# Kernel tuning notes

Measured on AMD Instinct MI355X. Metric: run time of the kernel, lower is better.

## Reference

```python
import jax, jax.numpy as jnp
from jax import lax
import numpy as np

GAMMA = 0.25        # inv_temp
C_SCALE = 1.0       # spectral_scale
STRIDE = 8          # patch stride (== patch_size, non-overlapping)


def setup_inputs() -> dict:
    key = jax.random.key(0)
    ks = jax.random.split(key, 9)
    B, C, H = 1024, 3, 64
    D, NP, M, NH, R, P = 256, 64, 1024, 8, 32, 8
    return {
        "x": jax.random.normal(ks[0], (B, C, H, H), jnp.float32),
        "z": jax.random.normal(ks[1], (B, NP, D), jnp.float32),
        "encoder_weight": jax.random.normal(ks[2], (D, C, P, P), jnp.float32) * 0.05,
        "encoder_bias": jax.random.normal(ks[3], (D,), jnp.float32) * 0.05,
        "visible_bias": jax.random.normal(ks[4], (C, H, H), jnp.float32) * 0.05,
        "pos_bias": jax.random.normal(ks[5], (NP, D), jnp.float32) * 0.05,
        "memory_weight": jax.random.normal(ks[6], (D, M), jnp.float32) * 0.05,
        "W_Q": jax.random.normal(ks[7], (NH, R, D), jnp.float32) * 0.05,
        "W_K": jax.random.normal(ks[8], (NH, R, D), jnp.float32) * 0.05,
    }


def reference(x, z, encoder_weight, encoder_bias, visible_bias, pos_bias,
              memory_weight, W_Q, W_K):
    """E = 0.5||x||^2 + 0.5||z||^2 - Phi_coupling(x, z); returns (B,)."""
    B = x.shape[0]
    D = encoder_weight.shape[0]

    quad_x = 0.5 * jnp.sum(x * x, axis=(1, 2, 3))
    quad_z = 0.5 * jnp.sum(z * z, axis=(1, 2))

    # visible-bias coupling
    phi_vis = jnp.sum(visible_bias[None] * x, axis=(1, 2, 3))

    # conv encode: (B, D, gh, gw) -> (B, NP, D)
    enc = lax.conv_general_dilated(
        x, C_SCALE * encoder_weight, window_strides=(STRIDE, STRIDE),
        padding='VALID', dimension_numbers=('NCHW', 'OIHW', 'NCHW'))
    encoded = enc.reshape(B, D, -1).transpose(0, 2, 1)  # (B, NP, D)

    # enc_act = 'none' -> identity
    phi_enc = jnp.sum(encoded * z, axis=(1, 2))
    phi_bias = jnp.sum(z * encoder_bias, axis=(1, 2))
    phi_pos = jnp.sum(z * pos_bias[None], axis=(1, 2))

    # memory ReLU^2 term: (B, NP, M)
    mem_proj = jnp.einsum('bpd,dm->bpm', z, C_SCALE * memory_weight)
    phi_mem = jnp.sum(jnp.square(jax.nn.relu(mem_proj)), axis=(1, 2))

    # Hopfield attention logsumexp term
    Q = jnp.einsum('bpd,hrd->bhrp', z, C_SCALE * W_Q)  # (B, H, R, NP)
    K = jnp.einsum('bpd,hrd->bhrp', z, C_SCALE * W_K)
    A = jnp.einsum('bhdm,bhdn->bhmn', Q, K)            # (B, H, NP, NP)
    phi_att = jnp.sum(jax.scipy.special.logsumexp(GAMMA * A, axis=-1),
                      axis=(1, 2)) / GAMMA

    coupling = phi_vis + phi_enc + phi_bias + phi_pos + phi_mem + phi_att
    return quad_x + quad_z - coupling
```

## Files before the change

kernel.cpp:

```cpp
#include <hip/hip_runtime.h>
#include <hip/hip_bf16.h>

#define GAMMA 0.25f


typedef __attribute__((ext_vector_type(8))) short short8;
typedef __attribute__((ext_vector_type(4))) float f32x4;

__device__ __forceinline__ float dot4(float4 a, float4 b) {
  return fmaf(a.x, b.x, fmaf(a.y, b.y, fmaf(a.z, b.z, a.w * b.w)));
}

__device__ __forceinline__ void fma4(float4& a, float s, float4 w) {
  a.x = fmaf(s, w.x, a.x); a.y = fmaf(s, w.y, a.y);
  a.z = fmaf(s, w.z, a.z); a.w = fmaf(s, w.w, a.w);
}

__device__ __forceinline__ ushort f2bf(float f) {
  __hip_bfloat16 h = __float2bfloat16(f);
  return *reinterpret_cast<ushort*>(&h);
}

__device__ __forceinline__ float bf2f(ushort u) {
  union { unsigned int i; float f; } v;
  v.i = ((unsigned int)u) << 16;
  return v.f;
}

__device__ __forceinline__ float block_sum_256(float v, float* tmp) {
#pragma unroll
  for (int off = 32; off; off >>= 1) v += __shfl_down(v, off, 64);
  int w = threadIdx.x >> 6;
  if ((threadIdx.x & 63) == 0) tmp[w] = v;
  __syncthreads();
  return tmp[0] + tmp[1] + tmp[2] + tmp[3];
}

__global__ __launch_bounds__(256) void k_cvt_weights_v4(
    const float* __restrict__ wq, const float* __restrict__ wk,
    const float* __restrict__ ew, const float* __restrict__ mw,
    ushort* __restrict__ wcf, ushort* __restrict__ ewt,
    ushort* __restrict__ mtf) {
  int bid = blockIdx.x, t = threadIdx.x;
  ushort o[8];
  if (bid < 64) {
    int tid = bid * 256 + t;
    int frag = tid >> 6, l = tid & 63;
    int ctg = frag >> 3, kc = frag & 7;
    int col = ctg * 16 + (l & 15);
    int h = col >> 6, qk = (col >> 5) & 1, rr = col & 31;
    int k0 = kc * 32 + (l >> 4) * 8;
    const float* s = (qk ? wk : wq) + ((size_t)h * 32 + rr) * 256 + k0;
#pragma unroll
    for (int i = 0; i < 8; ++i) o[i] = f2bf(s[i]);
    *(ushort4*)(wcf + (size_t)tid * 8) = *(ushort4*)&o[0];
    *(ushort4*)(wcf + (size_t)tid * 8 + 4) = *(ushort4*)&o[4];
  } else if (bid < 88) {
    int tid = (bid - 64) * 256 + t;
    int frag = tid >> 6, l = tid & 63;
    int ks = frag / 12, ct = frag % 12;
    const float* s = ew + (size_t)(ks * 32 + (l >> 4) * 8) * 192 +
                     ct * 16 + (l & 15);
#pragma unroll
    for (int i = 0; i < 8; ++i) o[i] = f2bf(s[(size_t)i * 192]);
    *(ushort4*)(ewt + (size_t)tid * 8) = *(ushort4*)&o[0];
    *(ushort4*)(ewt + (size_t)tid * 8 + 4) = *(ushort4*)&o[4];
  } else {
    int tid = (bid - 88) * 256 + t;
    int frag = tid >> 6, l = tid & 63;
    int C = frag >> 3, kc = frag & 7;
    int k0 = kc * 32 + (l >> 4) * 8, col = C * 16 + (l & 15);
#pragma unroll
    for (int i = 0; i < 8; ++i) o[i] = f2bf(mw[(size_t)(k0 + i) * 1024 + col]);
    *(ushort4*)(mtf + (size_t)tid * 8) = *(ushort4*)&o[0];
    *(ushort4*)(mtf + (size_t)tid * 8 + 4) = *(ushort4*)&o[4];
  }
}

__global__ __launch_bounds__(256) void k_mega(
    const float* __restrict__ z, const float* __restrict__ eb,
    const float* __restrict__ pb, const ushort* __restrict__ mtf,
    const ushort* __restrict__ wcf, float* __restrict__ out) {
  __shared__ ushort SL[32768];
  const int t = threadIdx.x, l = t & 63, w = t >> 6;
  const int b = blockIdx.x;
  const int q = l >> 4, m = l & 15;
  float s = 0.f;

  {
    const float4* zb4 = (const float4*)(z + (size_t)b * 16384);
    const float4* pb4 = (const float4*)pb;
    const float4* eb4 = (const float4*)eb;
#pragma unroll
    for (int n = 0; n < 16; ++n) {
      int i = t + n * 256;
      float4 zv = zb4[i];
      float4 pv = pb4[i];
      float4 ev = eb4[i & 63];
      float4 c;
      c.x = pv.x + ev.x; c.y = pv.y + ev.y;
      c.z = pv.z + ev.z; c.w = pv.w + ev.w;
      s += 0.5f * dot4(zv, zv) - dot4(zv, c);
      int p = i >> 6, d4 = i & 63;
      int ks = d4 >> 3, sub = (d4 & 7) >> 1, e0 = (d4 & 1) * 4;
      int li = (p & 15) + sub * 16;
      ushort4 o;
      o.x = f2bf(zv.x); o.y = f2bf(zv.y); o.z = f2bf(zv.z); o.w = f2bf(zv.w);
      *(ushort4*)(SL + (size_t)(((p >> 4) * 8 + ks) * 64 + li) * 8 + e0) = o;
    }
  }
  __syncthreads();

#pragma unroll 1
  for (int ctl = 0; ctl < 4; ++ctl) {
    const ushort* Bb = mtf + ((size_t)(ctl * 16 + w * 4) * 8) * 512 +
                       (size_t)l * 8;
    short8 fb[2][4];
#pragma unroll
    for (int c = 0; c < 4; ++c) fb[0][c] = *(const short8*)(Bb + (c * 8 + 0) * 512);
#pragma unroll
    for (int c = 0; c < 4; ++c) fb[1][c] = *(const short8*)(Bb + (c * 8 + 1) * 512);

    f32x4 acc[4][4];
#pragma unroll
    for (int r = 0; r < 4; ++r)
#pragma unroll
      for (int c = 0; c < 4; ++c) acc[r][c] = f32x4{0.f, 0.f, 0.f, 0.f};

#pragma unroll
    for (int kc = 0; kc < 8; ++kc) {
      const int cur = kc & 1;
      short8 a4[4];
#pragma unroll
      for (int r = 0; r < 4; ++r)
        a4[r] = *(const short8*)(SL + (size_t)((r * 8 + kc) * 64 + l) * 8);
#pragma unroll
      for (int r = 0; r < 4; ++r)
#pragma unroll
        for (int c = 0; c < 4; ++c)
          acc[r][c] = __builtin_amdgcn_mfma_f32_16x16x32_bf16(a4[r], fb[cur][c],
                                                              acc[r][c], 0, 0, 0);
      if (kc < 6) {
#pragma unroll
        for (int c = 0; c < 4; ++c)
          fb[cur][c] = *(const short8*)(Bb + (c * 8 + kc + 2) * 512);
      }
    }
#pragma unroll
    for (int r = 0; r < 4; ++r)
#pragma unroll
      for (int c = 0; c < 4; ++c)
#pragma unroll
        for (int e = 0; e < 4; ++e) {
          float rr = fmaxf(acc[r][c][e], 0.f);
          s -= rr * rr;
        }
  }

  float part = 0.f;
  char* dstg = (char*)(SL + 16384);
#pragma unroll 1
  for (int half = 0; half < 2; ++half) {
    const ushort* Bb = wcf + ((size_t)((half * 16 + w * 4) * 8)) * 512 +
                       (size_t)l * 8;
    short8 fb[2][4];
#pragma unroll
    for (int c = 0; c < 4; ++c) fb[0][c] = *(const short8*)(Bb + (c * 8 + 0) * 512);
#pragma unroll
    for (int c = 0; c < 4; ++c) fb[1][c] = *(const short8*)(Bb + (c * 8 + 1) * 512);

    f32x4 acc[4][4];
#pragma unroll
    for (int r = 0; r < 4; ++r)
#pragma unroll
      for (int c = 0; c < 4; ++c) acc[r][c] = f32x4{0.f, 0.f, 0.f, 0.f};

#pragma unroll
    for (int kc = 0; kc < 8; ++kc) {
      const int cur = kc & 1;
      short8 a4[4];
#pragma unroll
      for (int r = 0; r < 4; ++r)
        a4[r] = *(const short8*)(SL + (size_t)((r * 8 + kc) * 64 + l) * 8);
#pragma unroll
      for (int r = 0; r < 4; ++r)
#pragma unroll
        for (int c = 0; c < 4; ++c)
          acc[r][c] = __builtin_amdgcn_mfma_f32_16x16x32_bf16(a4[r], fb[cur][c],
                                                              acc[r][c], 0, 0, 0);
      if (kc < 6) {
#pragma unroll
        for (int c = 0; c < 4; ++c)
          fb[cur][c] = *(const short8*)(Bb + (c * 8 + kc + 2) * 512);
      }
    }

#pragma unroll
    for (int rt = 0; rt < 4; ++rt)
#pragma unroll
      for (int c = 0; c < 4; ++c)
#pragma unroll
        for (int reg = 0; reg < 4; ++reg) {
          int row = 16 * rt + 4 * q + reg;
          int col = (4 * w + c) * 16 + m;
          int ba = ((row * 256 + col) * 2) ^ ((row & 7) << 4);
          *(ushort*)(dstg + ba) = f2bf(acc[rt][c][reg]);
        }
    __syncthreads();

#pragma unroll
    for (int hh = 0; hh < 4; ++hh) {
      int rowq = 16 * w + m;
      short8 qa = *(const short8*)(
          dstg + (((rowq * 256 + hh * 64 + q * 8) * 2) ^ ((rowq & 7) << 4)));
      f32x4 a2[4];
#pragma unroll
      for (int nt = 0; nt < 4; ++nt) {
        int rowk = 16 * nt + m;
        short8 kb = *(const short8*)(
            dstg + (((rowk * 256 + hh * 64 + 32 + q * 8) * 2) ^ ((rowk & 7) << 4)));
        a2[nt] = __builtin_amdgcn_mfma_f32_16x16x32_bf16(
            qa, kb, f32x4{0.f, 0.f, 0.f, 0.f}, 0, 0, 0);
      }
#pragma unroll
      for (int reg = 0; reg < 4; ++reg) {
        float e = __expf(GAMMA * a2[0][reg]) + __expf(GAMMA * a2[1][reg]) +
                  __expf(GAMMA * a2[2][reg]) + __expf(GAMMA * a2[3][reg]);
        e += __shfl_xor(e, 1, 64);
        e += __shfl_xor(e, 2, 64);
        e += __shfl_xor(e, 4, 64);
        e += __shfl_xor(e, 8, 64);
        part += (m == 0) ? __logf(e) : 0.f;
      }
    }
    __syncthreads();
  }
  s -= part * (1.0f / GAMMA);

  float r = block_sum_256(s, (float*)SL);
  if (t == 0) out[b] = r;
}

__global__ __launch_bounds__(256) void k_enc_v5(
    const float* __restrict__ x, const float* __restrict__ vb,
    const float* __restrict__ z, const ushort* __restrict__ ewt,
    float* __restrict__ out) {
  __shared__ ushort xs[12288];
  __shared__ ushort ebuf[2][6144];
  __shared__ float tmp[4];
  const int b = blockIdx.x, t = threadIdx.x, l = t & 63, w = t >> 6;
  const int q = l >> 4, m = l & 15;

  const float* Zr = z + (size_t)b * 16384 + (size_t)(16 * w + m) * 256 + q * 8;
  short8 a[8];
#pragma unroll
  for (int ks = 0; ks < 8; ++ks) {
    float4 u = *(const float4*)(Zr + ks * 32);
    float4 v = *(const float4*)(Zr + ks * 32 + 4);
    ushort o[8];
    o[0] = f2bf(u.x); o[1] = f2bf(u.y); o[2] = f2bf(u.z); o[3] = f2bf(u.w);
    o[4] = f2bf(v.x); o[5] = f2bf(v.y); o[6] = f2bf(v.z); o[7] = f2bf(v.w);
    a[ks] = *(short8*)o;
  }

  short8 st[3];
#pragma unroll
  for (int i = 0; i < 3; ++i)
    st[i] = *(const short8*)(ewt + (size_t)(t + i * 256) * 8);

  const float4* xb = (const float4*)(x + (size_t)b * 12288);
  const float4* vb4 = (const float4*)vb;
  ushort4* xs4 = (ushort4*)xs;
  float s = 0.f;
  for (int i = t; i < 3072; i += 256) {
    float4 xv = xb[i];
    float4 bv = vb4[i];
    s += 0.5f * dot4(xv, xv) - dot4(bv, xv);
    ushort4 o;
    o.x = f2bf(xv.x); o.y = f2bf(xv.y); o.z = f2bf(xv.z); o.w = f2bf(xv.w);
    xs4[i] = o;
  }
#pragma unroll
  for (int i = 0; i < 3; ++i)
    *(short8*)(ebuf[0] + (size_t)(t + i * 256) * 8) = st[i];
  __syncthreads();

  f32x4 acc[12];
#pragma unroll
  for (int ct = 0; ct < 12; ++ct) acc[ct] = f32x4{0.f, 0.f, 0.f, 0.f};

#pragma unroll
  for (int ks = 0; ks < 8; ++ks) {
    const int cur = ks & 1;
    if (ks < 7) {
#pragma unroll
      for (int i = 0; i < 3; ++i)
        st[i] = *(const short8*)(ewt + (size_t)(ks + 1) * 6144 +
                                 (size_t)(t + i * 256) * 8);
    }
#pragma unroll
    for (int ct = 0; ct < 12; ++ct) {
      short8 bv = *(const short8*)(ebuf[cur] + (size_t)(ct * 64 + l) * 8);
      acc[ct] = __builtin_amdgcn_mfma_f32_16x16x32_bf16(a[ks], bv, acc[ct], 0, 0, 0);
    }
    if (ks < 7) {
#pragma unroll
      for (int i = 0; i < 3; ++i)
        *(short8*)(ebuf[cur ^ 1] + (size_t)(t + i * 256) * 8) = st[i];
    }
    __syncthreads();
  }

#pragma unroll
  for (int ct = 0; ct < 12; ++ct) {
#pragma unroll
    for (int reg = 0; reg < 4; ++reg) {
      const int p = 16 * w + 4 * q + reg, gi = p >> 3, gj = p & 7;
      const int k = ct * 16 + m, c = k >> 6, r2 = k & 63;
      const int ii = r2 >> 3, jj = r2 & 7;
      s -= acc[ct][reg] * bf2f(xs[c * 4096 + (gi * 8 + ii) * 64 + gj * 8 + jj]);
    }
  }
  float r = block_sum_256(s, tmp);
  if (t == 0) atomicAdd(out + b, r);
}

__global__ __launch_bounds__(256) void k_xz(const float* __restrict__ x,
                                            const float* __restrict__ z,
                                            const float* __restrict__ vb,
                                            const float* __restrict__ eb,
                                            const float* __restrict__ pb,
                                            float* __restrict__ out) {
  __shared__ float tmp[4];
  int b = blockIdx.x, t = threadIdx.x;
  const float4* xb = (const float4*)(x + (size_t)b * 12288);
  const float4* vb4 = (const float4*)vb;
  float s = 0.f;
  for (int i = t; i < 3072; i += 256) {
    float4 xv = xb[i];
    float4 bv = vb4[i];
    s += 0.5f * dot4(xv, xv) - dot4(bv, xv);
  }
  const float4* zb = (const float4*)(z + (size_t)b * 16384);
  const float4* pb4 = (const float4*)pb;
  const float4* eb4 = (const float4*)eb;
  for (int i = t; i < 4096; i += 256) {
    float4 zv = zb[i];
    float4 pv = pb4[i];
    float4 ev = eb4[i & 63];
    float4 c;
    c.x = pv.x + ev.x; c.y = pv.y + ev.y; c.z = pv.z + ev.z; c.w = pv.w + ev.w;
    s += 0.5f * dot4(zv, zv) - dot4(zv, c);
  }
  float r = block_sum_256(s, tmp);
  if (t == 0) out[b] = r;
}

__global__ __launch_bounds__(256) void k_enc(const float* __restrict__ x,
                                             const float* __restrict__ z,
                                             const float* __restrict__ ew,
                                             float* __restrict__ out) {
  __shared__ float xs[12288];
  __shared__ float tmp[4];
  int b = blockIdx.x, t = threadIdx.x;
  const float4* xb4 = (const float4*)(x + (size_t)b * 12288);
  for (int i = t; i < 3072; i += 256) ((float4*)xs)[i] = xb4[i];
  __syncthreads();

  float acc[64];
#pragma unroll
  for (int p = 0; p < 64; ++p) acc[p] = 0.f;

  for (int k4 = 0; k4 < 48; ++k4) {
    float4 wv = *(const float4*)(ew + (size_t)t * 192 + k4 * 4);
    int c = k4 >> 4;
    int ii = (k4 >> 1) & 7;
    int jh = (k4 & 1) * 4;
    const float* base = xs + c * 4096 + ii * 64 + jh;
#pragma unroll
    for (int p = 0; p < 64; ++p) {
      float4 pv = *(const float4*)(base + (p >> 3) * 512 + (p & 7) * 8);
      acc[p] = fmaf(wv.x, pv.x,
               fmaf(wv.y, pv.y, fmaf(wv.z, pv.z, fmaf(wv.w, pv.w, acc[p]))));
    }
  }
  const float* zb = z + (size_t)b * 16384;
  float s = 0.f;
#pragma unroll
  for (int p = 0; p < 64; ++p) s += acc[p] * zb[p * 256 + t];
  float r = block_sum_256(s, tmp);
  if (t == 0) atomicAdd(out + b, -r);
}

__global__ __launch_bounds__(256) void k_mem(const float* __restrict__ z,
                                             const float* __restrict__ mw,
                                             float* __restrict__ out) {
  __shared__ float zs[16 * 256];
  __shared__ float tmp[4];
  int b = blockIdx.x >> 2, pt = blockIdx.x & 3, t = threadIdx.x;
  const float4* zb4 = (const float4*)(z + (size_t)b * 16384 + pt * 4096);
  for (int i = t; i < 1024; i += 256) ((float4*)zs)[i] = zb4[i];
  __syncthreads();

  const float4* m4 = (const float4*)mw;
  float4 acc[16];
#pragma unroll
  for (int pp = 0; pp < 16; ++pp) acc[pp] = make_float4(0.f, 0.f, 0.f, 0.f);

#pragma unroll 2
  for (int k4 = 0; k4 < 64; ++k4) {
    float4 w0 = m4[(4 * k4 + 0) * 256 + t];
    float4 w1 = m4[(4 * k4 + 1) * 256 + t];
    float4 w2 = m4[(4 * k4 + 2) * 256 + t];
    float4 w3 = m4[(4 * k4 + 3) * 256 + t];
#pragma unroll
    for (int pp = 0; pp < 16; ++pp) {
      float4 zv = *(const float4*)&zs[pp * 256 + k4 * 4];
      fma4(acc[pp], zv.x, w0);
      fma4(acc[pp], zv.y, w1);
      fma4(acc[pp], zv.z, w2);
      fma4(acc[pp], zv.w, w3);
    }
  }
  float total = 0.f;
#pragma unroll
  for (int pp = 0; pp < 16; ++pp) {
    float r;
    r = fmaxf(acc[pp].x, 0.f); total = fmaf(r, r, total);
    r = fmaxf(acc[pp].y, 0.f); total = fmaf(r, r, total);
    r = fmaxf(acc[pp].z, 0.f); total = fmaf(r, r, total);
    r = fmaxf(acc[pp].w, 0.f); total = fmaf(r, r, total);
  }
  float r = block_sum_256(total, tmp);
  if (t == 0) atomicAdd(out + b, -r);
}

__global__ __launch_bounds__(256) void k_attn(const float* __restrict__ z,
                                              const float* __restrict__ wq,
                                              const float* __restrict__ wk,
                                              float* __restrict__ out) {
  __shared__ float lds[8192];
  __shared__ float red[4];
  const int b = blockIdx.x >> 1, half = blockIdx.x & 1;
  const int t = threadIdx.x;
  const int lane = t & 63;
  const int w = __builtin_amdgcn_readfirstlane(t >> 6);
  const float4* zb4 = (const float4*)(z + (size_t)b * 16384);

  float qa[4][8], ka[4][8];
#pragma unroll
  for (int hh = 0; hh < 4; ++hh)
#pragma unroll
    for (int j = 0; j < 8; ++j) { qa[hh][j] = 0.f; ka[hh][j] = 0.f; }

  float4* lds4 = (float4*)lds;
  for (int dc = 0; dc < 2; ++dc) {
    __syncthreads();
    for (int i = t; i < 2048; i += 256) {
      int p = i >> 5, ld4 = i & 31;
      lds4[ld4 * 64 + (p ^ (ld4 & 7))] = zb4[p * 64 + dc * 32 + ld4];
    }
    __syncthreads();
#pragma unroll
    for (int hh = 0; hh < 4; ++hh) {
      int h = half * 4 + hh;
      const float* Wqb = wq + (size_t)h * 8192 + (size_t)(w * 8) * 256 + dc * 128;
      const float* Wkb = wk + (size_t)h * 8192 + (size_t)(w * 8) * 256 + dc * 128;
      for (int ld4 = 0; ld4 < 32; ++ld4) {
        float4 wv[8], kv[8];
#pragma unroll
        for (int j = 0; j < 8; ++j) {
          wv[j] = *(const float4*)(Wqb + j * 256 + ld4 * 4);
          kv[j] = *(const float4*)(Wkb + j * 256 + ld4 * 4);
        }
        float4 zv = lds4[ld4 * 64 + (lane ^ (ld4 & 7))];
#pragma unroll
        for (int j = 0; j < 8; ++j) {
          qa[hh][j] = fmaf(wv[j].x, zv.x, fmaf(wv[j].y, zv.y,
                      fmaf(wv[j].z, zv.z, fmaf(wv[j].w, zv.w, qa[hh][j]))));
          ka[hh][j] = fmaf(kv[j].x, zv.x, fmaf(kv[j].y, zv.y,
                      fmaf(kv[j].z, zv.z, fmaf(kv[j].w, zv.w, ka[hh][j]))));
        }
      }
    }
  }

  float* Qs = lds;
  float* Ks = lds + 2048;
  float lse = 0.f;
#pragma unroll
  for (int hh = 0; hh < 4; ++hh) {
    __syncthreads();
#pragma unroll
    for (int j = 0; j < 8; ++j) {
      Qs[(w * 8 + j) * 64 + lane] = qa[hh][j];
      Ks[(w * 8 + j) * 64 + lane] = ka[hh][j];
    }
    __syncthreads();
    float av[16];
#pragma unroll
    for (int mm = 0; mm < 16; ++mm) av[mm] = 0.f;
    for (int rr = 0; rr < 32; ++rr) {
      float kv = Ks[rr * 64 + lane];
      const float* qrow = &Qs[rr * 64 + w * 16];
      float4 q0 = *(const float4*)(qrow + 0);
      float4 q1 = *(const float4*)(qrow + 4);
      float4 q2 = *(const float4*)(qrow + 8);
      float4 q3 = *(const float4*)(qrow + 12);
      av[0]  = fmaf(q0.x, kv, av[0]);  av[1]  = fmaf(q0.y, kv, av[1]);
      av[2]  = fmaf(q0.z, kv, av[2]);  av[3]  = fmaf(q0.w, kv, av[3]);
      av[4]  = fmaf(q1.x, kv, av[4]);  av[5]  = fmaf(q1.y, kv, av[5]);
      av[6]  = fmaf(q1.z, kv, av[6]);  av[7]  = fmaf(q1.w, kv, av[7]);
      av[8]  = fmaf(q2.x, kv, av[8]);  av[9]  = fmaf(q2.y, kv, av[9]);
      av[10] = fmaf(q2.z, kv, av[10]); av[11] = fmaf(q2.w, kv, av[11]);
      av[12] = fmaf(q3.x, kv, av[12]); av[13] = fmaf(q3.y, kv, av[13]);
      av[14] = fmaf(q3.z, kv, av[14]); av[15] = fmaf(q3.w, kv, av[15]);
    }
#pragma unroll
    for (int mm = 0; mm < 16; ++mm) {
      float e = __expf(GAMMA * av[mm]);
#pragma unroll
      for (int off = 32; off; off >>= 1) e += __shfl_xor(e, off, 64);
      lse += __logf(e);
    }
  }
  if (lane == 0) red[w] = lse;
  __syncthreads();
  if (t == 0)
    atomicAdd(out + b, -(red[0] + red[1] + red[2] + red[3]) * (1.0f / GAMMA));
}

extern "C" void kernel_launch(void* const* d_in, const int* in_sizes, int n_in,
                              void* d_out, int out_size, void* d_ws,
                              size_t ws_size, hipStream_t stream) {
  (void)in_sizes; (void)n_in; (void)out_size;
  const float* x  = (const float*)d_in[0];
  const float* z  = (const float*)d_in[1];
  const float* ew = (const float*)d_in[2];
  const float* eb = (const float*)d_in[3];
  const float* vb = (const float*)d_in[4];
  const float* pb = (const float*)d_in[5];
  const float* mw = (const float*)d_in[6];
  const float* wq = (const float*)d_in[7];
  const float* wk = (const float*)d_in[8];
  float* out = (float*)d_out;

  const size_t MT_B = (size_t)1024 * 256 * 2;
  const size_t WC_B = (size_t)512 * 256 * 2;
  const size_t EW_B = (size_t)96 * 64 * 8 * 2;
  const size_t FULL = MT_B + WC_B + EW_B;

  ushort* mtf = (ushort*)d_ws;
  ushort* wcf = (ushort*)((char*)d_ws + MT_B);
  ushort* ewt = (ushort*)((char*)d_ws + MT_B + WC_B);

  if (ws_size >= FULL) {
    k_cvt_weights_v4<<<216, 256, 0, stream>>>(wq, wk, ew, mw, wcf, ewt, mtf);
    k_mega  <<<1024, 256, 0, stream>>>(z, eb, pb, mtf, wcf, out);
    k_enc_v5<<<1024, 256, 0, stream>>>(x, vb, z, ewt, out);
  } else {
    k_xz  <<<1024, 256, 0, stream>>>(x, z, vb, eb, pb, out);
    k_enc <<<1024, 256, 0, stream>>>(x, z, ew, out);
    k_mem <<<4096, 256, 0, stream>>>(z, mw, out);
    k_attn<<<2048, 256, 0, stream>>>(z, wq, wk, out);
  }
}
```

Before: 222.4 us.

## Shrink attention staging to half the heads per pass, raise occupancy in k_mega

Cuts the shared memory of the fused z kernel to 48KB by staging Q/K for two heads per pass (four passes instead of two). This halves the accumulator tile, which lowers register pressure, and launch bounds now ask for three blocks per CU. The bf16 z tile moves to a row-major layout with an XOR swizzle, and the reduction scratch gets its own buffer. More passes mean more barriers and repeated A-fragment loads from LDS, and the output may not end up in the right place if the write in the kernel still uses the wrong address.

After: 300.8 us. 1.35x slower.

```diff
diff --git a/kernel.cpp b/kernel.cpp
--- a/kernel.cpp
+++ b/kernel.cpp
@@ -6,6 +6,9 @@
 
 typedef __attribute__((ext_vector_type(8))) short short8;
 typedef __attribute__((ext_vector_type(4))) float f32x4;
+
+#define ZS_SWZ(a) ((a) ^ ((((a) >> 9) & 7) << 4))
+#define DG_SWZ(a) ((a) ^ ((((a) >> 8) & 7) << 4))
 
 __device__ __forceinline__ float dot4(float4 a, float4 b) {
   return fmaf(a.x, b.x, fmaf(a.y, b.y, fmaf(a.z, b.z, a.w * b.w)));
@@ -25,6 +28,13 @@
   union { unsigned int i; float f; } v;
   v.i = ((unsigned int)u) << 16;
   return v.f;
+}
+
+__device__ __forceinline__ short8 zs_frag(const char* zsb, int rt, int kc,
+                                          int l) {
+  int row = 16 * rt + (l & 15);
+  int ba = row * 512 + (kc * 32 + (l >> 4) * 8) * 2;
+  return *(const short8*)(zsb + ZS_SWZ(ba));
 }
 
 __device__ __forceinline__ float block_sum_256(float v, float* tmp) {
@@ -77,11 +87,14 @@
   }
 }
 
-__global__ __launch_bounds__(256) void k_mega(
+__global__ __launch_bounds__(256, 3) void k_mega2(
     const float* __restrict__ z, const float* __restrict__ eb,
     const float* __restrict__ pb, const ushort* __restrict__ mtf,
     const ushort* __restrict__ wcf, float* __restrict__ out) {
-  __shared__ ushort SL[32768];
+  __shared__ char SL[49152];
+  __shared__ float tmp[4];
+  char* zsb = SL;
+  char* dgb = SL + 32768;
   const int t = threadIdx.x, l = t & 63, w = t >> 6;
   const int b = blockIdx.x;
   const int q = l >> 4, m = l & 15;
@@ -102,18 +115,17 @@
       c.z = pv.z + ev.z; c.w = pv.w + ev.w;
       s += 0.5f * dot4(zv, zv) - dot4(zv, c);
       int p = i >> 6, d4 = i & 63;
-      int ks = d4 >> 3, sub = (d4 & 7) >> 1, e0 = (d4 & 1) * 4;
-      int li = (p & 15) + sub * 16;
+      int ba = p * 512 + d4 * 8;
       ushort4 o;
       o.x = f2bf(zv.x); o.y = f2bf(zv.y); o.z = f2bf(zv.z); o.w = f2bf(zv.w);
-      *(ushort4*)(SL + (size_t)(((p >> 4) * 8 + ks) * 64 + li) * 8 + e0) = o;
+      *(ushort4*)(zsb + ZS_SWZ(ba)) = o;
     }
   }
   __syncthreads();
 
 #pragma unroll 1
-  for (int ctl = 0; ctl < 4; ++ctl) {
-    const ushort* Bb = mtf + ((size_t)(ctl * 16 + w * 4) * 8) * 512 +
+  for (int ct = 0; ct < 4; ++ct) {
+    const ushort* Bb = mtf + ((size_t)(ct * 16 + w * 4) * 8) * 512 +
                        (size_t)l * 8;
     short8 fb[2][4];
 #pragma unroll
@@ -132,8 +144,7 @@
       const int cur = kc & 1;
       short8 a4[4];
 #pragma unroll
-      for (int r = 0; r < 4; ++r)
-        a4[r] = *(const short8*)(SL + (size_t)((r * 8 + kc) * 64 + l) * 8);
+      for (int r = 0; r < 4; ++r) a4[r] = zs_frag(zsb, r, kc, l);
 #pragma unroll
       for (int r = 0; r < 4; ++r)
 #pragma unroll
@@ -158,39 +169,37 @@
   }
 
   float part = 0.f;
-  char* dstg = (char*)(SL + 16384);
 #pragma unroll 1
-  for (int half = 0; half < 2; ++half) {
-    const ushort* Bb = wcf + ((size_t)((half * 16 + w * 4) * 8)) * 512 +
+  for (int hp = 0; hp < 4; ++hp) {
+    const ushort* Bb = wcf + ((size_t)((hp * 8 + w * 2) * 8)) * 512 +
                        (size_t)l * 8;
-    short8 fb[2][4];
-#pragma unroll
-    for (int c = 0; c < 4; ++c) fb[0][c] = *(const short8*)(Bb + (c * 8 + 0) * 512);
-#pragma unroll
-    for (int c = 0; c < 4; ++c) fb[1][c] = *(const short8*)(Bb + (c * 8 + 1) * 512);
-
-    f32x4 acc[4][4];
+    short8 fb[2][2];
+#pragma unroll
+    for (int c = 0; c < 2; ++c) fb[0][c] = *(const short8*)(Bb + (c * 8 + 0) * 512);
+#pragma unroll
+    for (int c = 0; c < 2; ++c) fb[1][c] = *(const short8*)(Bb + (c * 8 + 1) * 512);
+
+    f32x4 acc[4][2];
 #pragma unroll
     for (int r = 0; r < 4; ++r)
 #pragma unroll
-      for (int c = 0; c < 4; ++c) acc[r][c] = f32x4{0.f, 0.f, 0.f, 0.f};
+      for (int c = 0; c < 2; ++c) acc[r][c] = f32x4{0.f, 0.f, 0.f, 0.f};
 
 #pragma unroll
     for (int kc = 0; kc < 8; ++kc) {
       const int cur = kc & 1;
       short8 a4[4];
 #pragma unroll
+      for (int r = 0; r < 4; ++r) a4[r] = zs_frag(zsb, r, kc, l);
+#pragma unroll
       for (int r = 0; r < 4; ++r)
-        a4[r] = *(const short8*)(SL + (size_t)((r * 8 + kc) * 64 + l) * 8);
-#pragma unroll
-      for (int r = 0; r < 4; ++r)
-#pragma unroll
-        for (int c = 0; c < 4; ++c)
+#pragma unroll
+        for (int c = 0; c < 2; ++c)
           acc[r][c] = __builtin_amdgcn_mfma_f32_16x16x32_bf16(a4[r], fb[cur][c],
                                                               acc[r][c], 0, 0, 0);
       if (kc < 6) {
 #pragma unroll
-        for (int c = 0; c < 4; ++c)
+        for (int c = 0; c < 2; ++c)
           fb[cur][c] = *(const short8*)(Bb + (c * 8 + kc + 2) * 512);
       }
     }
@@ -198,29 +207,29 @@
 #pragma unroll
     for (int rt = 0; rt < 4; ++rt)
 #pragma unroll
-      for (int c = 0; c < 4; ++c)
+      for (int c = 0; c < 2; ++c)
 #pragma unroll
         for (int reg = 0; reg < 4; ++reg) {
           int row = 16 * rt + 4 * q + reg;
-          int col = (4 * w + c) * 16 + m;
-          int ba = ((row * 256 + col) * 2) ^ ((row & 7) << 4);
-          *(ushort*)(dstg + ba) = f2bf(acc[rt][c][reg]);
+          int lc = (2 * w + c) * 16 + m;
+          int ba = row * 256 + lc * 2;
+          *(ushort*)(dgb + DG_SWZ(ba)) = f2bf(acc[rt][c][reg]);
         }
     __syncthreads();
 
 #pragma unroll
-    for (int hh = 0; hh < 4; ++hh) {
+    for (int hh = 0; hh < 2; ++hh) {
       int rowq = 16 * w + m;
       short8 qa = *(const short8*)(
-          dstg + (((rowq * 256 + hh * 64 + q * 8) * 2) ^ ((rowq & 7) << 4)));
+          dgb + DG_SWZ(rowq * 256 + (hh * 64 + q * 8) * 2));
       f32x4 a2[4];
 #pragma unroll
       for (int nt = 0; nt < 4; ++nt) {
         int rowk = 16 * nt + m;
-        short8 kb = *(const short8*)(
-            dstg + (((rowk * 256 + hh * 64 + 32 + q * 8) * 2) ^ ((rowk & 7) << 4)));
         a2[nt] = __builtin_amdgcn_mfma_f32_16x16x32_bf16(
-            qa, kb, f32x4{0.f, 0.f, 0.f, 0.f}, 0, 0, 0);
+            qa,
+            *(const short8*)(dgb + DG_SWZ(rowk * 256 + (hh * 64 + 32 + q * 8) * 2)),
+            f32x4{0.f, 0.f, 0.f, 0.f}, 0, 0, 0);
       }
 #pragma unroll
       for (int reg = 0; reg < 4; ++reg) {
@@ -237,7 +246,7 @@
   }
   s -= part * (1.0f / GAMMA);
 
-  float r = block_sum_256(s, (float*)SL);
+  float r = block_sum_256(s, tmp);
   if (t == 0) out[b] = r;
 }
 
@@ -556,7 +565,7 @@
 
   if (ws_size >= FULL) {
     k_cvt_weights_v4<<<216, 256, 0, stream>>>(wq, wk, ew, mw, wcf, ewt, mtf);
-    k_mega  <<<1024, 256, 0, stream>>>(z, eb, pb, mtf, wcf, out);
+    k_mega2 <<<1024, 256, 0, stream>>>(z, eb, pb, mtf, wcf, out);
     k_enc_v5<<<1024, 256, 0, stream>>>(x, vb, z, ewt, out);
   } else {
     k_xz  <<<1024, 256, 0, stream>>>(x, z, vb, eb, pb, out);
```

## Fuse encoder-conv kernel into memory/attention mega kernel, reuse bf16 z from LDS

Applied to the files above, without the earlier changes.

Merges the separate encoder-convolution kernel into the memory/attention kernel, so one launch per batch row handles all terms. The bf16 z fragments already staged in shared memory are reused as MFMA A operands instead of reloading and reconverting z from global memory. The existing LDS buffer is aliased for the encoder weight double-buffer and the x tile, and the output is written directly rather than atomically added. This removes one launch, a second read of z and the atomic, but lengthens each block and may raise register pressure, lowering occupancy.

New measurement: 261.3 us. +17.5%, slower.

```diff
diff --git a/kernel.cpp b/kernel.cpp
--- a/kernel.cpp
+++ b/kernel.cpp
@@ -77,10 +77,12 @@
   }
 }
 
-__global__ __launch_bounds__(256) void k_mega(
-    const float* __restrict__ z, const float* __restrict__ eb,
-    const float* __restrict__ pb, const ushort* __restrict__ mtf,
-    const ushort* __restrict__ wcf, float* __restrict__ out) {
+__global__ __launch_bounds__(256) void k_omega(
+    const float* __restrict__ x, const float* __restrict__ z,
+    const float* __restrict__ eb, const float* __restrict__ vb,
+    const float* __restrict__ pb, const ushort* __restrict__ ewt,
+    const ushort* __restrict__ mtf, const ushort* __restrict__ wcf,
+    float* __restrict__ out) {
   __shared__ ushort SL[32768];
   const int t = threadIdx.x, l = t & 63, w = t >> 6;
   const int b = blockIdx.x;
@@ -112,8 +114,8 @@
   __syncthreads();
 
 #pragma unroll 1
-  for (int ctl = 0; ctl < 4; ++ctl) {
-    const ushort* Bb = mtf + ((size_t)(ctl * 16 + w * 4) * 8) * 512 +
+  for (int ct = 0; ct < 4; ++ct) {
+    const ushort* Bb = mtf + ((size_t)(ct * 16 + w * 4) * 8) * 512 +
                        (size_t)l * 8;
     short8 fb[2][4];
 #pragma unroll
@@ -237,52 +239,34 @@
   }
   s -= part * (1.0f / GAMMA);
 
-  float r = block_sum_256(s, (float*)SL);
-  if (t == 0) out[b] = r;
-}
-
-__global__ __launch_bounds__(256) void k_enc_v5(
-    const float* __restrict__ x, const float* __restrict__ vb,
-    const float* __restrict__ z, const ushort* __restrict__ ewt,
-    float* __restrict__ out) {
-  __shared__ ushort xs[12288];
-  __shared__ ushort ebuf[2][6144];
-  __shared__ float tmp[4];
-  const int b = blockIdx.x, t = threadIdx.x, l = t & 63, w = t >> 6;
-  const int q = l >> 4, m = l & 15;
-
-  const float* Zr = z + (size_t)b * 16384 + (size_t)(16 * w + m) * 256 + q * 8;
-  short8 a[8];
-#pragma unroll
-  for (int ks = 0; ks < 8; ++ks) {
-    float4 u = *(const float4*)(Zr + ks * 32);
-    float4 v = *(const float4*)(Zr + ks * 32 + 4);
-    ushort o[8];
-    o[0] = f2bf(u.x); o[1] = f2bf(u.y); o[2] = f2bf(u.z); o[3] = f2bf(u.w);
-    o[4] = f2bf(v.x); o[5] = f2bf(v.y); o[6] = f2bf(v.z); o[7] = f2bf(v.w);
-    a[ks] = *(short8*)o;
-  }
-
+  short8 ae[8];
+#pragma unroll
+  for (int ks = 0; ks < 8; ++ks)
+    ae[ks] = *(const short8*)(SL + (size_t)((w * 8 + ks) * 64 + l) * 8);
   short8 st[3];
 #pragma unroll
-  for (int i = 0; i < 3; ++i)
-    st[i] = *(const short8*)(ewt + (size_t)(t + i * 256) * 8);
+  for (int i2 = 0; i2 < 3; ++i2)
+    st[i2] = *(const short8*)(ewt + (size_t)(t + i2 * 256) * 8);
+  __syncthreads();
+
+  ushort* ebuf0 = SL;
+  ushort* ebuf1 = SL + 6144;
+  ushort* xs    = SL + 16384;
 
   const float4* xb = (const float4*)(x + (size_t)b * 12288);
   const float4* vb4 = (const float4*)vb;
   ushort4* xs4 = (ushort4*)xs;
-  float s = 0.f;
-  for (int i = t; i < 3072; i += 256) {
-    float4 xv = xb[i];
-    float4 bv = vb4[i];
+  for (int i2 = t; i2 < 3072; i2 += 256) {
+    float4 xv = xb[i2];
+    float4 bv = vb4[i2];
     s += 0.5f * dot4(xv, xv) - dot4(bv, xv);
     ushort4 o;
     o.x = f2bf(xv.x); o.y = f2bf(xv.y); o.z = f2bf(xv.z); o.w = f2bf(xv.w);
-    xs4[i] = o;
-  }
-#pragma unroll
-  for (int i = 0; i < 3; ++i)
-    *(short8*)(ebuf[0] + (size_t)(t + i * 256) * 8) = st[i];
+    xs4[i2] = o;
+  }
+#pragma unroll
+  for (int i2 = 0; i2 < 3; ++i2)
+    *(short8*)(ebuf0 + (size_t)(t + i2 * 256) * 8) = st[i2];
   __syncthreads();
 
   f32x4 acc[12];
@@ -291,22 +275,23 @@
 
 #pragma unroll
   for (int ks = 0; ks < 8; ++ks) {
-    const int cur = ks & 1;
+    ushort* eb_cur = (ks & 1) ? ebuf1 : ebuf0;
+    ushort* eb_nxt = (ks & 1) ? ebuf0 : ebuf1;
     if (ks < 7) {
 #pragma unroll
-      for (int i = 0; i < 3; ++i)
-        st[i] = *(const short8*)(ewt + (size_t)(ks + 1) * 6144 +
-                                 (size_t)(t + i * 256) * 8);
+      for (int i2 = 0; i2 < 3; ++i2)
+        st[i2] = *(const short8*)(ewt + (size_t)(ks + 1) * 6144 +
+                                  (size_t)(t + i2 * 256) * 8);
     }
 #pragma unroll
     for (int ct = 0; ct < 12; ++ct) {
-      short8 bv = *(const short8*)(ebuf[cur] + (size_t)(ct * 64 + l) * 8);
-      acc[ct] = __builtin_amdgcn_mfma_f32_16x16x32_bf16(a[ks], bv, acc[ct], 0, 0, 0);
+      short8 bv = *(const short8*)(eb_cur + (size_t)(ct * 64 + l) * 8);
+      acc[ct] = __builtin_amdgcn_mfma_f32_16x16x32_bf16(ae[ks], bv, acc[ct], 0, 0, 0);
     }
     if (ks < 7) {
 #pragma unroll
-      for (int i = 0; i < 3; ++i)
-        *(short8*)(ebuf[cur ^ 1] + (size_t)(t + i * 256) * 8) = st[i];
+      for (int i2 = 0; i2 < 3; ++i2)
+        *(short8*)(eb_nxt + (size_t)(t + i2 * 256) * 8) = st[i2];
     }
     __syncthreads();
   }
@@ -321,8 +306,9 @@
       s -= acc[ct][reg] * bf2f(xs[c * 4096 + (gi * 8 + ii) * 64 + gj * 8 + jj]);
     }
   }
-  float r = block_sum_256(s, tmp);
-  if (t == 0) atomicAdd(out + b, r);
+
+  float r = block_sum_256(s, (float*)SL);
+  if (t == 0) out[b] = r;
 }
 
 __global__ __launch_bounds__(256) void k_xz(const float* __restrict__ x,
@@ -556,8 +542,7 @@
 
   if (ws_size >= FULL) {
     k_cvt_weights_v4<<<216, 256, 0, stream>>>(wq, wk, ew, mw, wcf, ewt, mtf);
-    k_mega  <<<1024, 256, 0, stream>>>(z, eb, pb, mtf, wcf, out);
-    k_enc_v5<<<1024, 256, 0, stream>>>(x, vb, z, ewt, out);
+    k_omega<<<1024, 256, 0, stream>>>(x, z, eb, vb, pb, ewt, mtf, wcf, out);
   } else {
     k_xz  <<<1024, 256, 0, stream>>>(x, z, vb, eb, pb, out);
     k_enc <<<1024, 256, 0, stream>>>(x, z, ew, out);
```
